# Kernel optimization log

Hardware: AMD Instinct MI355X
Metric: run time of the kernel (lower is better)

The kernel has to match this reference:

```python
import jax, jax.numpy as jnp
import numpy as np


def _layernorm(x, gamma, beta, eps=1e-5):
    mu = jnp.mean(x, axis=-1, keepdims=True)
    var = jnp.mean(jnp.square(x - mu), axis=-1, keepdims=True)
    return (x - mu) * jax.lax.rsqrt(var + eps) * gamma + beta


def _sparse_ternary_linear(x, W, b, sparsity):
    # Ternary quantization (BitNet-style): per-tensor scale = mean(|W|),
    # dynamic sparsity: zero out the `sparsity` fraction of smallest-|W| entries,
    # remaining weights -> sign(W), rescaled by `scale`.
    absW = jnp.abs(W)
    scale = jnp.mean(absW)
    thresh = jnp.quantile(absW, sparsity)
    q = jnp.sign(W) * (absW > thresh).astype(W.dtype)  # ternary {-1,0,+1}
    return jnp.einsum('bnd,hd->bnh', x, q * scale) + b


def setup_inputs() -> dict:
    key = jax.random.key(0)
    ks = jax.random.split(key, 8)
    B, N, D, H = 32, 1024, 768, 3072
    return {
        'x': jax.random.normal(ks[0], (B, N, D), dtype=jnp.float32),
        'ln1_g': jnp.ones((D,), jnp.float32),
        'ln1_b': jnp.zeros((D,), jnp.float32),
        'W1': jax.random.normal(ks[1], (H, D), dtype=jnp.float32) * 0.02,
        'b1': jnp.zeros((H,), jnp.float32),
        'ln2_g': jnp.ones((H,), jnp.float32),
        'ln2_b': jnp.zeros((H,), jnp.float32),
        'W2': jax.random.normal(ks[2], (D, H), dtype=jnp.float32) * 0.02,
        'b2': jnp.zeros((D,), jnp.float32),
        'sparsity': jnp.float32(0.5),
    }


def reference(x, ln1_g, ln1_b, W1, b1, ln2_g, ln2_b, W2, b2, sparsity):
    h = _layernorm(x, ln1_g, ln1_b)
    h = _sparse_ternary_linear(h, W1, b1, sparsity)
    h = jax.nn.gelu(h)  # dropout=0.0 (eval): identity
    h = _layernorm(h, ln2_g, ln2_b)
    h = _sparse_ternary_linear(h, W2, b2, sparsity)
    return h
```

## Files before the change

### kernel.cpp

```cpp
#include <hip/hip_runtime.h>
#include <math.h>

using f32x4    = __attribute__((ext_vector_type(4))) float;
using short8   = __attribute__((ext_vector_type(8))) short;
using ushort8  = __attribute__((ext_vector_type(8))) unsigned short;
using ushort4v = __attribute__((ext_vector_type(4))) unsigned short;
using u32x4    = __attribute__((ext_vector_type(4))) unsigned int;

#define D_DIM 768
#define H_DIM 3072

#define L1_BITS 14
#define L1_SIZE 16384

static const size_t HIST1_OFF = 0;
static const size_t HIST2_OFF = 131072;
static const size_t HIST3_OFF = 139264;
static const size_t SUM_OFF   = 147456;
static const size_t THR_OFF   = 147472;
static const size_t META_OFF  = 147488;
static const size_t ZERO_BYTES= 147616;
static const size_t WQ1_OFF   = 5242880;
static const size_t WQ2_OFF   = WQ1_OFF + 4718592;
static const size_t H1_OFF    = 16777216;


__device__ __forceinline__ unsigned short f2bf(float f) {
    unsigned u = __float_as_uint(f);
    u += 0x7fffu + ((u >> 16) & 1u);
    return (unsigned short)(u >> 16);
}
__device__ __forceinline__ float bf2f(unsigned short s) {
    return __uint_as_float(((unsigned)s) << 16);
}

__device__ __forceinline__ void gload16(const unsigned short* g, unsigned short* l) {
    __builtin_amdgcn_global_load_lds(
        (const __attribute__((address_space(1))) unsigned int*)g,
        (__attribute__((address_space(3))) unsigned int*)l, 16, 0, 0);
}

__global__ void hist_abs_kernel(const float* __restrict__ W1, int n1,
                                const float* __restrict__ W2, int n2,
                                unsigned* __restrict__ hist, double* __restrict__ sums) {
    __shared__ unsigned lh[L1_SIZE];
    const int t = blockIdx.y;
    const float* W = t ? W2 : W1;
    const int n = t ? n2 : n1;
    unsigned* hg = hist + (size_t)t * L1_SIZE;

    for (int i = threadIdx.x; i < L1_SIZE; i += 256) lh[i] = 0;
    __syncthreads();

    int tid = blockIdx.x * blockDim.x + threadIdx.x;
    int stride = gridDim.x * blockDim.x;
    double local = 0.0;
    int n4 = n >> 2;
    for (int i = tid; i < n4; i += stride) {
        f32x4 w = ((const f32x4*)W)[i];
#pragma unroll
        for (int j = 0; j < 4; j++) {
            float a = fabsf(w[j]);
            local += (double)a;
            atomicAdd(&lh[__float_as_uint(a) >> (32 - L1_BITS)], 1u);
        }
    }
    for (int i = (n4 << 2) + tid; i < n; i += stride) {
        float a = fabsf(W[i]);
        local += (double)a;
        atomicAdd(&lh[__float_as_uint(a) >> (32 - L1_BITS)], 1u);
    }
    __syncthreads();
    for (int i = threadIdx.x; i < L1_SIZE; i += 256) {
        unsigned c = lh[i];
        if (c) atomicAdd(&hg[i], c);
    }
#pragma unroll
    for (int off = 32; off >= 1; off >>= 1) local += __shfl_down(local, off);
    if ((threadIdx.x & 63) == 0) atomicAdd(&sums[t], local);
}

__global__ void scan1_kernel(const unsigned* __restrict__ hist, unsigned* __restrict__ meta_u,
                             const float* __restrict__ sparsity, int n1, int n2) {
    __shared__ unsigned partial[256];
    __shared__ unsigned basearr[256];
    for (int t = 0; t < 2; t++) {
        const unsigned* h = hist + (size_t)t * L1_SIZE;
        int n = t ? n2 : n1;
        double p = (double)(*sparsity) * (double)(n - 1);
        unsigned kA = (unsigned)floor(p);
        unsigned kB = kA + 1; if (kB > (unsigned)(n - 1)) kB = (unsigned)(n - 1);
        int b0 = threadIdx.x * 64;
        unsigned s_local = 0;
#pragma unroll
        for (int b = 0; b < 64; b += 4) {
            u32x4 v = *(const u32x4*)&h[b0 + b];
            s_local += v[0] + v[1] + v[2] + v[3];
        }
        partial[threadIdx.x] = s_local;
        __syncthreads();
        if (threadIdx.x == 0) {
            unsigned run = 0;
            for (int i = 0; i < 256; i++) { unsigned tmp = partial[i]; basearr[i] = run; run += tmp; }
        }
        __syncthreads();
        unsigned cumbase = basearr[threadIdx.x];
        for (int s = 0; s < 2; s++) {
            unsigned rank = s ? kB : kA;
            if (rank >= cumbase && rank < cumbase + s_local) {
                unsigned cum = cumbase;
                for (int b = 0; b < 64; b++) {
                    unsigned c = h[b0 + b];
                    if (rank < cum + c) { meta_u[s * 4 + t] = (unsigned)(b0 + b); meta_u[s * 4 + 2 + t] = rank - cum; break; }
                    cum += c;
                }
            }
        }
        __syncthreads();
    }
}

template<int LVL>
__global__ void histN_kernel(const float* __restrict__ W1, int n1,
                             const float* __restrict__ W2, int n2,
                             const unsigned* __restrict__ meta_u, unsigned* __restrict__ histo) {
    __shared__ unsigned hA[512], hB[512];
    const int t = blockIdx.y;
    const float* W = t ? W2 : W1;
    const int n = t ? n2 : n1;
    for (int i = threadIdx.x; i < 512; i += 256) { hA[i] = 0; hB[i] = 0; }
    __syncthreads();
    const int inbase = (LVL == 2) ? 0 : 16;
    unsigned pa = meta_u[inbase + 0 + t], pb = meta_u[inbase + 4 + t];
    int tid = blockIdx.x * blockDim.x + threadIdx.x;
    int stride = gridDim.x * blockDim.x;
    int n4 = n >> 2;
    for (int i = tid; i < n4; i += stride) {
        f32x4 w = ((const f32x4*)W)[i];
#pragma unroll
        for (int j = 0; j < 4; j++) {
            unsigned u = __float_as_uint(fabsf(w[j]));
            unsigned pf  = (LVL == 2) ? (u >> 18) : (u >> 9);
            unsigned idx = (LVL == 2) ? ((u >> 9) & 0x1FFu) : (u & 0x1FFu);
            if (pf == pa) atomicAdd(&hA[idx], 1u);
            if (pf == pb) atomicAdd(&hB[idx], 1u);
        }
    }
    for (int i = (n4 << 2) + tid; i < n; i += stride) {
        unsigned u = __float_as_uint(fabsf(W[i]));
        unsigned pf  = (LVL == 2) ? (u >> 18) : (u >> 9);
        unsigned idx = (LVL == 2) ? ((u >> 9) & 0x1FFu) : (u & 0x1FFu);
        if (pf == pa) atomicAdd(&hA[idx], 1u);
        if (pf == pb) atomicAdd(&hB[idx], 1u);
    }
    __syncthreads();
    for (int i = threadIdx.x; i < 512; i += 256) {
        unsigned a = hA[i]; if (a) atomicAdd(&histo[(size_t)(t * 2 + 0) * 512 + i], a);
        unsigned b = hB[i]; if (b) atomicAdd(&histo[(size_t)(t * 2 + 1) * 512 + i], b);
    }
}

__global__ void scan_mid_kernel(const unsigned* __restrict__ histo, unsigned* __restrict__ meta_u) {
    int wave = threadIdx.x >> 6, lane = threadIdx.x & 63;
    int s = wave >> 1, t = wave & 1;
    const unsigned* h = histo + (size_t)(t * 2 + s) * 512;
    unsigned rank = meta_u[s * 4 + 2 + t];
    unsigned pfx  = meta_u[s * 4 + t];
    u32x4 ca = *(const u32x4*)&h[lane * 8];
    u32x4 cb = *(const u32x4*)&h[lane * 8 + 4];
    unsigned cc[8] = {ca[0], ca[1], ca[2], ca[3], cb[0], cb[1], cb[2], cb[3]};
    unsigned csum = cc[0] + cc[1] + cc[2] + cc[3] + cc[4] + cc[5] + cc[6] + cc[7];
    unsigned inc = csum;
#pragma unroll
    for (int off = 1; off < 64; off <<= 1) {
        unsigned v = __shfl_up(inc, off, 64);
        if (lane >= off) inc += v;
    }
    unsigned pre = inc - csum;
    if (rank >= pre && rank < pre + csum) {
        unsigned cum = pre, rem = 0, bucket = 0; bool found = false;
#pragma unroll
        for (int j = 0; j < 8; j++) {
            if (!found) {
                if (rank < cum + cc[j]) { bucket = lane * 8 + j; rem = rank - cum; found = true; }
                else cum += cc[j];
            }
        }
        meta_u[16 + s * 4 + t] = (pfx << 9) | bucket;
        meta_u[16 + s * 4 + 2 + t] = rem;
    }
}

__global__ void scan_fin_kernel(const unsigned* __restrict__ histo, unsigned* __restrict__ meta_u,
                                const double* __restrict__ sums, const float* __restrict__ sparsity,
                                double* __restrict__ thr, int n1, int n2) {
    __shared__ unsigned vbs[4];
    int wave = threadIdx.x >> 6, lane = threadIdx.x & 63;
    int s = wave >> 1, t = wave & 1;
    const unsigned* h = histo + (size_t)(t * 2 + s) * 512;
    unsigned rank = meta_u[16 + s * 4 + 2 + t];
    unsigned pfx  = meta_u[16 + s * 4 + t];
    u32x4 ca = *(const u32x4*)&h[lane * 8];
    u32x4 cb = *(const u32x4*)&h[lane * 8 + 4];
    unsigned cc[8] = {ca[0], ca[1], ca[2], ca[3], cb[0], cb[1], cb[2], cb[3]};
    unsigned csum = cc[0] + cc[1] + cc[2] + cc[3] + cc[4] + cc[5] + cc[6] + cc[7];
    unsigned inc = csum;
#pragma unroll
    for (int off = 1; off < 64; off <<= 1) {
        unsigned v = __shfl_up(inc, off, 64);
        if (lane >= off) inc += v;
    }
    unsigned pre = inc - csum;
    if (rank >= pre && rank < pre + csum) {
        unsigned cum = pre, bucket = 0; bool found = false;
#pragma unroll
        for (int j = 0; j < 8; j++) {
            if (!found) {
                if (rank < cum + cc[j]) { bucket = lane * 8 + j; found = true; }
                else cum += cc[j];
            }
        }
        vbs[t * 2 + s] = (pfx << 9) | bucket;
    }
    __syncthreads();
    if (threadIdx.x < 2) {
        int tt = threadIdx.x;
        int n = tt ? n2 : n1;
        double a = (double)__uint_as_float(vbs[tt * 2 + 0]);
        double b = (double)__uint_as_float(vbs[tt * 2 + 1]);
        double p = (double)(*sparsity) * (double)(n - 1);
        double tfr = p - floor(p);
        double th = (tfr >= 0.5) ? (b - (b - a) * (1.0 - tfr)) : (a + (b - a) * tfr);
        thr[tt] = th;
        ((float*)meta_u)[24 + tt] = (float)(sums[tt] / (double)n);
    }
}

__global__ void quantize_kernel(const float* __restrict__ W1, int n1,
                                const float* __restrict__ W2, int n2,
                                const double* __restrict__ thr,
                                unsigned short* __restrict__ wq1, unsigned short* __restrict__ wq2) {
    int tid = blockIdx.x * blockDim.x + threadIdx.x;
    int stride = gridDim.x * blockDim.x;
    for (int t = 0; t < 2; t++) {
        const float* W = t ? W2 : W1;
        unsigned short* O = t ? wq2 : wq1;
        int n = t ? n2 : n1;
        double th = thr[t];
        int n4 = n >> 2;
        for (int i = tid; i < n4; i += stride) {
            f32x4 w = ((const f32x4*)W)[i];
            ushort4v q;
#pragma unroll
            for (int j = 0; j < 4; j++) {
                float a = fabsf(w[j]);
                unsigned short v = 0;
                if ((double)a > th) v = (w[j] > 0.f) ? 0x3F80u : 0xBF80u;
                q[j] = v;
            }
            ((ushort4v*)O)[i] = q;
        }
        for (int i = (n4 << 2) + tid; i < n; i += stride) {
            float wv = W[i];
            float a = fabsf(wv);
            unsigned short v = 0;
            if ((double)a > th) v = (wv > 0.f) ? 0x3F80u : 0xBF80u;
            O[i] = v;
        }
    }
}

__global__ void ln1_apply_kernel(const float* __restrict__ x, const float* __restrict__ g,
                                 const float* __restrict__ b, unsigned short* __restrict__ xn, int M) {
    int wave = threadIdx.x >> 6, lane = threadIdx.x & 63;
    int row = blockIdx.x * 4 + wave;
    if (row >= M) return;
    const float* xr = x + (size_t)row * D_DIM;
    f32x4 xv[3];
    float s = 0.f, s2 = 0.f;
#pragma unroll
    for (int i = 0; i < 3; i++) {
        xv[i] = *(const f32x4*)&xr[lane * 4 + i * 256];
#pragma unroll
        for (int j = 0; j < 4; j++) { s += xv[i][j]; s2 += xv[i][j] * xv[i][j]; }
    }
#pragma unroll
    for (int off = 32; off >= 1; off >>= 1) { s += __shfl_xor(s, off); s2 += __shfl_xor(s2, off); }
    float m = s / (float)D_DIM;
    float var = s2 / (float)D_DIM - m * m;
    float rs = 1.f / sqrtf(var + 1e-5f);
    unsigned short* xo = xn + (size_t)row * D_DIM;
#pragma unroll
    for (int i = 0; i < 3; i++) {
        int k = lane * 4 + i * 256;
        f32x4 gg = *(const f32x4*)&g[k];
        f32x4 bb = *(const f32x4*)&b[k];
        ushort4v o;
#pragma unroll
        for (int j = 0; j < 4; j++) o[j] = f2bf((xv[i][j] - m) * rs * gg[j] + bb[j]);
        *(ushort4v*)&xo[k] = o;
    }
}

__global__ void ln2_fuse_kernel(unsigned short* __restrict__ h1, const float* __restrict__ g,
                                const float* __restrict__ b, int M) {
    int wave = threadIdx.x >> 6, lane = threadIdx.x & 63;
    int row = blockIdx.x * 4 + wave;
    if (row >= M) return;
    unsigned short* hr = h1 + (size_t)row * H_DIM;
    ushort8 hv[6];
    float s = 0.f, s2 = 0.f;
#pragma unroll
    for (int i = 0; i < 6; i++) {
        hv[i] = *(const ushort8*)&hr[lane * 8 + i * 512];
#pragma unroll
        for (int j = 0; j < 8; j++) { float f = bf2f(hv[i][j]); s += f; s2 += f * f; }
    }
#pragma unroll
    for (int off = 32; off >= 1; off >>= 1) { s += __shfl_xor(s, off); s2 += __shfl_xor(s2, off); }
    float m = s / (float)H_DIM;
    float var = s2 / (float)H_DIM - m * m;
    float rs = 1.f / sqrtf(var + 1e-5f);
#pragma unroll
    for (int i = 0; i < 6; i++) {
        int k = lane * 8 + i * 512;
        f32x4 ga = *(const f32x4*)&g[k];
        f32x4 gb = *(const f32x4*)&g[k + 4];
        f32x4 ba = *(const f32x4*)&b[k];
        f32x4 bb = *(const f32x4*)&b[k + 4];
        ushort8 o;
#pragma unroll
        for (int j = 0; j < 4; j++) o[j]     = f2bf((bf2f(hv[i][j])     - m) * rs * ga[j] + ba[j]);
#pragma unroll
        for (int j = 0; j < 4; j++) o[4 + j] = f2bf((bf2f(hv[i][4 + j]) - m) * rs * gb[j] + bb[j]);
        *(ushort8*)&hr[k] = o;
    }
}

template<int KD, int EPI>
__launch_bounds__(256)
__global__ void gemm_tern_kernel(const unsigned short* __restrict__ A,
                                 const unsigned short* __restrict__ Bq,
                                 const float* __restrict__ bias,
                                 const float* __restrict__ meta_f, int sidx,
                                 void* __restrict__ outp) {
    __shared__ unsigned short As[128 * 64];
    __shared__ unsigned short Bs[128 * 64];
    const int m0 = blockIdx.y * 128, n0 = blockIdx.x * 128;
    const float scale = meta_f[sidx];
    const int tt = threadIdx.x, lane = tt & 63, wave = tt >> 6;
    const int wm = (wave & 1) * 64, wn = (wave >> 1) * 64;
    const int l16 = lane & 15, l4 = lane >> 4;
    const int srow = tt >> 3, schunk = tt & 7;

    f32x4 acc[4][4];
#pragma unroll
    for (int mi = 0; mi < 4; mi++)
#pragma unroll
        for (int ni = 0; ni < 4; ni++) acc[mi][ni] = (f32x4){0.f, 0.f, 0.f, 0.f};

    for (int k0 = 0; k0 < KD; k0 += 64) {
#pragma unroll
        for (int r = 0; r < 4; r++) {
            int row = r * 32 + srow;
            int sc = (schunk ^ (row & 7)) << 3;
            gload16(&A[(size_t)(m0 + row) * KD + k0 + sc], &As[(size_t)tt * 8 + r * 2048]);
        }
#pragma unroll
        for (int r = 0; r < 4; r++) {
            int row = r * 32 + srow;
            int sc = (schunk ^ (row & 7)) << 3;
            gload16(&Bq[(size_t)(n0 + row) * KD + k0 + sc], &Bs[(size_t)tt * 8 + r * 2048]);
        }
        __syncthreads();
#pragma unroll
        for (int ks = 0; ks < 2; ks++) {
            short8 af[4], bf_[4];
#pragma unroll
            for (int i = 0; i < 4; i++) {
                int ar = wm + i * 16 + l16;
                af[i] = *(const short8*)&As[ar * 64 + (((ks * 4 + l4) ^ (ar & 7)) << 3)];
                int br = wn + i * 16 + l16;
                bf_[i] = *(const short8*)&Bs[br * 64 + (((ks * 4 + l4) ^ (br & 7)) << 3)];
            }
#pragma unroll
            for (int mi = 0; mi < 4; mi++)
#pragma unroll
                for (int ni = 0; ni < 4; ni++)
                    acc[mi][ni] = __builtin_amdgcn_mfma_f32_16x16x32_bf16(af[mi], bf_[ni], acc[mi][ni], 0, 0, 0);
        }
        __syncthreads();
    }

#pragma unroll
    for (int ni = 0; ni < 4; ni++) {
        int col = n0 + wn + ni * 16 + l16;
        float bl = bias[col];
#pragma unroll
        for (int mi = 0; mi < 4; mi++) {
#pragma unroll
            for (int j = 0; j < 4; j++) {
                int row = m0 + wm + mi * 16 + l4 * 4 + j;
                float v = acc[mi][ni][j] * scale + bl;
                if constexpr (EPI == 1) {
                    float y = 1.5957691216f * (v + 0.044715f * v * v * v);
                    float e = exp2f(-1.4426950409f * y);
                    float gel = v / (1.f + e);
                    ((unsigned short*)outp)[(size_t)row * H_DIM + col] = f2bf(gel);
                } else {
                    ((float*)outp)[(size_t)row * D_DIM + col] = v;
                }
            }
        }
    }
}

extern "C" void kernel_launch(void* const* d_in, const int* in_sizes, int n_in,
                              void* d_out, int out_size, void* d_ws, size_t ws_size,
                              hipStream_t stream) {
    const float* x    = (const float*)d_in[0];
    const float* ln1g = (const float*)d_in[1];
    const float* ln1b = (const float*)d_in[2];
    const float* W1   = (const float*)d_in[3];
    const float* b1   = (const float*)d_in[4];
    const float* ln2g = (const float*)d_in[5];
    const float* ln2b = (const float*)d_in[6];
    const float* W2   = (const float*)d_in[7];
    const float* b2   = (const float*)d_in[8];
    const float* sp   = (const float*)d_in[9];
    const int n1 = in_sizes[3], n2 = in_sizes[7];
    const int M = in_sizes[0] / D_DIM;

    char* ws = (char*)d_ws;
    unsigned* hist1 = (unsigned*)(ws + HIST1_OFF);
    unsigned* hist2 = (unsigned*)(ws + HIST2_OFF);
    unsigned* hist3 = (unsigned*)(ws + HIST3_OFF);
    double*   sums  = (double*)(ws + SUM_OFF);
    double*   thr   = (double*)(ws + THR_OFF);
    unsigned* meta_u = (unsigned*)(ws + META_OFF);
    float*    meta_f = (float*)(ws + META_OFF);
    unsigned short* wq1 = (unsigned short*)(ws + WQ1_OFF);
    unsigned short* wq2 = (unsigned short*)(ws + WQ2_OFF);
    unsigned short* h1  = (unsigned short*)(ws + H1_OFF);
    unsigned short* xn  = (unsigned short*)d_out;

    hipMemsetAsync(d_ws, 0, ZERO_BYTES, stream);
    hist_abs_kernel<<<dim3(512, 2), 256, 0, stream>>>(W1, n1, W2, n2, hist1, sums);
    scan1_kernel<<<1, 256, 0, stream>>>(hist1, meta_u, sp, n1, n2);
    histN_kernel<2><<<dim3(256, 2), 256, 0, stream>>>(W1, n1, W2, n2, meta_u, hist2);
    scan_mid_kernel<<<1, 256, 0, stream>>>(hist2, meta_u);
    histN_kernel<3><<<dim3(256, 2), 256, 0, stream>>>(W1, n1, W2, n2, meta_u, hist3);
    scan_fin_kernel<<<1, 256, 0, stream>>>(hist3, meta_u, sums, sp, thr, n1, n2);
    quantize_kernel<<<2048, 256, 0, stream>>>(W1, n1, W2, n2, thr, wq1, wq2);
    ln1_apply_kernel<<<M / 4, 256, 0, stream>>>(x, ln1g, ln1b, xn, M);
    gemm_tern_kernel<D_DIM, 1><<<dim3(H_DIM / 128, M / 128), 256, 0, stream>>>(xn, wq1, b1, meta_f, 24, h1);
    ln2_fuse_kernel<<<M / 4, 256, 0, stream>>>(h1, ln2g, ln2b, M);
    gemm_tern_kernel<H_DIM, 2><<<dim3(D_DIM / 128, M / 128), 256, 0, stream>>>(h1, wq2, b2, meta_f, 25, d_out);
}
```

Baseline: 792.8 us.

## Fold LayerNorm2 into GEMM epilogues via row stats and gamma-scaled ternary weights

Removes the separate ln2 pass over the bf16 hidden activation. GEMM1 now accumulates per-row sum and sum-of-squares with atomics in its epilogue. Gamma is folded into the quantized W2 and the mean and beta terms are applied through precomputed column sums in GEMM2's epilogue. It also remaps block IDs so consecutive blocks on each XCD share M tiles. The cost is the atomics, a small stats kernel, and GEMM2 consuming un-normalized bf16 activations, which changes numerics (variance via E[x^2]-m^2, mean subtraction after the product).

```diff
diff --git a/kernel.cpp b/kernel.cpp
--- a/kernel.cpp
+++ b/kernel.cpp
@@ -19,11 +19,16 @@
 static const size_t SUM_OFF   = 147456;
 static const size_t THR_OFF   = 147472;
 static const size_t META_OFF  = 147488;
-static const size_t ZERO_BYTES= 147616;
+static const size_t MU2A_OFF  = 147616;
+static const size_t SS2A_OFF  = 278688;
+static const size_t ZERO_BYTES= 409760;
+static const size_t S1_OFF    = 409760;
+static const size_t S2_OFF    = 412832;
+static const size_t MU2_OFF   = 415904;
+static const size_t RS2_OFF   = 546976;
 static const size_t WQ1_OFF   = 5242880;
-static const size_t WQ2_OFF   = WQ1_OFF + 4718592;
+static const size_t WQ2_OFF   = 9961472;
 static const size_t H1_OFF    = 16777216;
-
 
 __device__ __forceinline__ unsigned short f2bf(float f) {
     unsigned u = __float_as_uint(f);
@@ -238,7 +243,7 @@
 
 __global__ void quantize_kernel(const float* __restrict__ W1, int n1,
                                 const float* __restrict__ W2, int n2,
-                                const double* __restrict__ thr,
+                                const double* __restrict__ thr, const float* __restrict__ g2,
                                 unsigned short* __restrict__ wq1, unsigned short* __restrict__ wq2) {
     int tid = blockIdx.x * blockDim.x + threadIdx.x;
     int stride = gridDim.x * blockDim.x;
@@ -251,23 +256,55 @@
         for (int i = tid; i < n4; i += stride) {
             f32x4 w = ((const f32x4*)W)[i];
             ushort4v q;
-#pragma unroll
-            for (int j = 0; j < 4; j++) {
-                float a = fabsf(w[j]);
-                unsigned short v = 0;
-                if ((double)a > th) v = (w[j] > 0.f) ? 0x3F80u : 0xBF80u;
-                q[j] = v;
+            if (t == 0) {
+#pragma unroll
+                for (int j = 0; j < 4; j++) {
+                    unsigned short v = 0;
+                    if ((double)fabsf(w[j]) > th) v = (w[j] > 0.f) ? 0x3F80u : 0xBF80u;
+                    q[j] = v;
+                }
+            } else {
+                int k4 = (i % (H_DIM / 4)) * 4;
+                f32x4 g = *(const f32x4*)&g2[k4];
+#pragma unroll
+                for (int j = 0; j < 4; j++) {
+                    unsigned short v = 0;
+                    if ((double)fabsf(w[j]) > th) {
+                        unsigned short gb = f2bf(g[j]);
+                        v = (w[j] > 0.f) ? gb : (unsigned short)(gb ^ 0x8000u);
+                    }
+                    q[j] = v;
+                }
             }
             ((ushort4v*)O)[i] = q;
         }
-        for (int i = (n4 << 2) + tid; i < n; i += stride) {
-            float wv = W[i];
-            float a = fabsf(wv);
-            unsigned short v = 0;
-            if ((double)a > th) v = (wv > 0.f) ? 0x3F80u : 0xBF80u;
-            O[i] = v;
-        }
-    }
+    }
+}
+
+__global__ void colsum_kernel(const float* __restrict__ W2, const double* __restrict__ thr,
+                              const float* __restrict__ g2, const float* __restrict__ bln2,
+                              float* __restrict__ S1, float* __restrict__ S2) {
+    int wave = threadIdx.x >> 6, lane = threadIdx.x & 63;
+    int c = blockIdx.x * 4 + wave;
+    const float* wr = W2 + (size_t)c * H_DIM;
+    double th = thr[1];
+    float s1 = 0.f, s2 = 0.f;
+    for (int k = lane * 4; k < H_DIM; k += 256) {
+        f32x4 w = *(const f32x4*)&wr[k];
+        f32x4 g = *(const f32x4*)&g2[k];
+        f32x4 b = *(const f32x4*)&bln2[k];
+#pragma unroll
+        for (int j = 0; j < 4; j++) {
+            if ((double)fabsf(w[j]) > th) {
+                float sg = (w[j] > 0.f) ? 1.f : -1.f;
+                s1 += sg * bf2f(f2bf(g[j]));
+                s2 += sg * b[j];
+            }
+        }
+    }
+#pragma unroll
+    for (int off = 32; off >= 1; off >>= 1) { s1 += __shfl_xor(s1, off); s2 += __shfl_xor(s2, off); }
+    if (lane == 0) { S1[c] = s1; S2[c] = s2; }
 }
 
 __global__ void ln1_apply_kernel(const float* __restrict__ x, const float* __restrict__ g,
@@ -302,51 +339,33 @@
     }
 }
 
-__global__ void ln2_fuse_kernel(unsigned short* __restrict__ h1, const float* __restrict__ g,
-                                const float* __restrict__ b, int M) {
-    int wave = threadIdx.x >> 6, lane = threadIdx.x & 63;
-    int row = blockIdx.x * 4 + wave;
-    if (row >= M) return;
-    unsigned short* hr = h1 + (size_t)row * H_DIM;
-    ushort8 hv[6];
-    float s = 0.f, s2 = 0.f;
-#pragma unroll
-    for (int i = 0; i < 6; i++) {
-        hv[i] = *(const ushort8*)&hr[lane * 8 + i * 512];
-#pragma unroll
-        for (int j = 0; j < 8; j++) { float f = bf2f(hv[i][j]); s += f; s2 += f * f; }
-    }
-#pragma unroll
-    for (int off = 32; off >= 1; off >>= 1) { s += __shfl_xor(s, off); s2 += __shfl_xor(s2, off); }
-    float m = s / (float)H_DIM;
-    float var = s2 / (float)H_DIM - m * m;
-    float rs = 1.f / sqrtf(var + 1e-5f);
-#pragma unroll
-    for (int i = 0; i < 6; i++) {
-        int k = lane * 8 + i * 512;
-        f32x4 ga = *(const f32x4*)&g[k];
-        f32x4 gb = *(const f32x4*)&g[k + 4];
-        f32x4 ba = *(const f32x4*)&b[k];
-        f32x4 bb = *(const f32x4*)&b[k + 4];
-        ushort8 o;
-#pragma unroll
-        for (int j = 0; j < 4; j++) o[j]     = f2bf((bf2f(hv[i][j])     - m) * rs * ga[j] + ba[j]);
-#pragma unroll
-        for (int j = 0; j < 4; j++) o[4 + j] = f2bf((bf2f(hv[i][4 + j]) - m) * rs * gb[j] + bb[j]);
-        *(ushort8*)&hr[k] = o;
-    }
-}
-
-template<int KD, int EPI>
+__global__ void ln2stats_kernel(const float* __restrict__ sa, const float* __restrict__ sb,
+                                float* __restrict__ mu, float* __restrict__ rs, int M) {
+    int i = blockIdx.x * 256 + threadIdx.x;
+    if (i >= M) return;
+    float m = sa[i] / (float)H_DIM;
+    float var = sb[i] / (float)H_DIM - m * m;
+    mu[i] = m;
+    rs[i] = 1.f / sqrtf(var + 1e-5f);
+}
+
+template<int KD, int NBN, int EPI>
 __launch_bounds__(256)
 __global__ void gemm_tern_kernel(const unsigned short* __restrict__ A,
                                  const unsigned short* __restrict__ Bq,
                                  const float* __restrict__ bias,
                                  const float* __restrict__ meta_f, int sidx,
-                                 void* __restrict__ outp) {
+                                 void* __restrict__ outp,
+                                 float* __restrict__ rsum_g, float* __restrict__ rsum2_g,
+                                 const float* __restrict__ mu2, const float* __restrict__ rs2,
+                                 const float* __restrict__ S1, const float* __restrict__ S2) {
     __shared__ unsigned short As[128 * 64];
     __shared__ unsigned short Bs[128 * 64];
-    const int m0 = blockIdx.y * 128, n0 = blockIdx.x * 128;
+    const int bid = blockIdx.x;
+    const int xcd = bid & 7, idx = bid >> 3;
+    const int mb = (idx / NBN) * 8 + xcd;
+    const int nb = idx % NBN;
+    const int m0 = mb * 128, n0 = nb * 128;
     const float scale = meta_f[sidx];
     const int tt = threadIdx.x, lane = tt & 63, wave = tt >> 6;
     const int wm = (wave & 1) * 64, wn = (wave >> 1) * 64;
@@ -392,26 +411,59 @@
         __syncthreads();
     }
 
-#pragma unroll
-    for (int ni = 0; ni < 4; ni++) {
-        int col = n0 + wn + ni * 16 + l16;
-        float bl = bias[col];
-#pragma unroll
-        for (int mi = 0; mi < 4; mi++) {
-#pragma unroll
-            for (int j = 0; j < 4; j++) {
-                int row = m0 + wm + mi * 16 + l4 * 4 + j;
-                float v = acc[mi][ni][j] * scale + bl;
-                if constexpr (EPI == 1) {
+    if constexpr (EPI == 1) {
+        float rs_[4][4], rq_[4][4];
+#pragma unroll
+        for (int mi = 0; mi < 4; mi++)
+#pragma unroll
+            for (int j = 0; j < 4; j++) { rs_[mi][j] = 0.f; rq_[mi][j] = 0.f; }
+#pragma unroll
+        for (int ni = 0; ni < 4; ni++) {
+            int col = n0 + wn + ni * 16 + l16;
+            float bl = bias[col];
+#pragma unroll
+            for (int mi = 0; mi < 4; mi++)
+#pragma unroll
+                for (int j = 0; j < 4; j++) {
+                    int row = m0 + wm + mi * 16 + l4 * 4 + j;
+                    float v = acc[mi][ni][j] * scale + bl;
                     float y = 1.5957691216f * (v + 0.044715f * v * v * v);
                     float e = exp2f(-1.4426950409f * y);
                     float gel = v / (1.f + e);
-                    ((unsigned short*)outp)[(size_t)row * H_DIM + col] = f2bf(gel);
-                } else {
+                    unsigned short hb = f2bf(gel);
+                    float gv = bf2f(hb);
+                    ((unsigned short*)outp)[(size_t)row * H_DIM + col] = hb;
+                    rs_[mi][j] += gv;
+                    rq_[mi][j] += gv * gv;
+                }
+        }
+#pragma unroll
+        for (int mi = 0; mi < 4; mi++)
+#pragma unroll
+            for (int j = 0; j < 4; j++) {
+                float s = rs_[mi][j], q = rq_[mi][j];
+#pragma unroll
+                for (int off = 1; off <= 8; off <<= 1) { s += __shfl_xor(s, off); q += __shfl_xor(q, off); }
+                if (l16 == 0) {
+                    int row = m0 + wm + mi * 16 + l4 * 4 + j;
+                    atomicAdd(&rsum_g[row], s);
+                    atomicAdd(&rsum2_g[row], q);
+                }
+            }
+    } else {
+#pragma unroll
+        for (int mi = 0; mi < 4; mi++)
+#pragma unroll
+            for (int j = 0; j < 4; j++) {
+                int row = m0 + wm + mi * 16 + l4 * 4 + j;
+                float mr = mu2[row], rr = rs2[row];
+#pragma unroll
+                for (int ni = 0; ni < 4; ni++) {
+                    int col = n0 + wn + ni * 16 + l16;
+                    float v = scale * (rr * (acc[mi][ni][j] - mr * S1[col]) + S2[col]) + bias[col];
                     ((float*)outp)[(size_t)row * D_DIM + col] = v;
                 }
             }
-        }
     }
 }
 
@@ -439,6 +491,12 @@
     double*   thr   = (double*)(ws + THR_OFF);
     unsigned* meta_u = (unsigned*)(ws + META_OFF);
     float*    meta_f = (float*)(ws + META_OFF);
+    float* mu2a = (float*)(ws + MU2A_OFF);
+    float* ss2a = (float*)(ws + SS2A_OFF);
+    float* S1   = (float*)(ws + S1_OFF);
+    float* S2   = (float*)(ws + S2_OFF);
+    float* mu2  = (float*)(ws + MU2_OFF);
+    float* rs2  = (float*)(ws + RS2_OFF);
     unsigned short* wq1 = (unsigned short*)(ws + WQ1_OFF);
     unsigned short* wq2 = (unsigned short*)(ws + WQ2_OFF);
     unsigned short* h1  = (unsigned short*)(ws + H1_OFF);
@@ -451,9 +509,12 @@
     scan_mid_kernel<<<1, 256, 0, stream>>>(hist2, meta_u);
     histN_kernel<3><<<dim3(256, 2), 256, 0, stream>>>(W1, n1, W2, n2, meta_u, hist3);
     scan_fin_kernel<<<1, 256, 0, stream>>>(hist3, meta_u, sums, sp, thr, n1, n2);
-    quantize_kernel<<<2048, 256, 0, stream>>>(W1, n1, W2, n2, thr, wq1, wq2);
+    quantize_kernel<<<2048, 256, 0, stream>>>(W1, n1, W2, n2, thr, ln2g, wq1, wq2);
+    colsum_kernel<<<D_DIM / 4, 256, 0, stream>>>(W2, thr, ln2g, ln2b, S1, S2);
     ln1_apply_kernel<<<M / 4, 256, 0, stream>>>(x, ln1g, ln1b, xn, M);
-    gemm_tern_kernel<D_DIM, 1><<<dim3(H_DIM / 128, M / 128), 256, 0, stream>>>(xn, wq1, b1, meta_f, 24, h1);
-    ln2_fuse_kernel<<<M / 4, 256, 0, stream>>>(h1, ln2g, ln2b, M);
-    gemm_tern_kernel<H_DIM, 2><<<dim3(D_DIM / 128, M / 128), 256, 0, stream>>>(h1, wq2, b2, meta_f, 25, d_out);
-}
+    gemm_tern_kernel<D_DIM, 24, 1><<<24 * (M / 128), 256, 0, stream>>>(
+        xn, wq1, b1, meta_f, 24, h1, mu2a, ss2a, nullptr, nullptr, nullptr, nullptr);
+    ln2stats_kernel<<<M / 256, 256, 0, stream>>>(mu2a, ss2a, mu2, rs2, M);
+    gemm_tern_kernel<H_DIM, 6, 2><<<6 * (M / 128), 256, 0, stream>>>(
+        h1, wq2, b2, meta_f, 25, d_out, nullptr, nullptr, mu2, rs2, S1, S2);
+}
```

After: 987.8 us. 24.6% more time.
